# Kernel optimization log

Hardware: AMD Instinct MI355X
Metric: run time of the kernel (lower is better)

Reference implementation:

```python
import jax, jax.numpy as jnp
import numpy as np

N, E, G = 100000, 400000, 4096
H, C = 4, 32            # heads, hidden_dim per head
D_OUT = H * C           # 128
NODE_D, EDGE_D = 38, 13
DEC_H, OUT_D = 64, 1
NEG_SLOPE = 0.2
LN_EPS = 1e-5


def setup_inputs() -> dict:
    key = jax.random.key(0)
    ks = jax.random.split(key, 40)
    r = lambda k, s: jax.random.normal(k, s, jnp.float32) * 0.1
    inp = {
        "x": jax.random.normal(ks[0], (N, NODE_D), jnp.float32),
        "edge_index": jax.random.randint(ks[1], (2, E), 0, N),
        "edge_attr": jax.random.uniform(ks[2], (E, EDGE_D), jnp.float32),
        "batch": jnp.sort(jax.random.randint(ks[3], (N,), 0, G)),
        # --- block 1 (in=38) ---
        "Wl1": r(ks[4], (NODE_D, D_OUT)), "bl1": jnp.zeros((D_OUT,), jnp.float32),
        "Wr1": r(ks[5], (NODE_D, D_OUT)), "br1": jnp.zeros((D_OUT,), jnp.float32),
        "We1": r(ks[6], (EDGE_D, D_OUT)),
        "att1": r(ks[7], (H, C)), "ab1": jnp.zeros((D_OUT,), jnp.float32),
        "ln_g1": jnp.ones((D_OUT,), jnp.float32), "ln_b1": jnp.zeros((D_OUT,), jnp.float32),
        "Wres": r(ks[8], (NODE_D, D_OUT)), "bres": jnp.zeros((D_OUT,), jnp.float32),
        # --- block 2 (in=128, residual = identity) ---
        "Wl2": r(ks[9], (D_OUT, D_OUT)), "bl2": jnp.zeros((D_OUT,), jnp.float32),
        "Wr2": r(ks[10], (D_OUT, D_OUT)), "br2": jnp.zeros((D_OUT,), jnp.float32),
        "We2": r(ks[11], (EDGE_D, D_OUT)),
        "att2": r(ks[12], (H, C)), "ab2": jnp.zeros((D_OUT,), jnp.float32),
        "ln_g2": jnp.ones((D_OUT,), jnp.float32), "ln_b2": jnp.zeros((D_OUT,), jnp.float32),
        # --- readout MLP ---
        "Wd1": r(ks[13], (D_OUT, DEC_H)), "bd1": jnp.zeros((DEC_H,), jnp.float32),
        "Wd2": r(ks[14], (DEC_H, OUT_D)), "bd2": jnp.zeros((OUT_D,), jnp.float32),
    }
    return inp


def _segment_softmax(logits, seg, n):
    m = jax.ops.segment_max(logits, seg, num_segments=n)
    ex = jnp.exp(logits - m[seg])
    s = jax.ops.segment_sum(ex, seg, num_segments=n)
    return ex / s[seg]


def _gatv2(x, src, dst, e_feat, Wl, bl, Wr, br, We, att, ab):
    n = x.shape[0]
    xl = (x @ Wl + bl).reshape(n, H, C)   # source transform
    xr = (x @ Wr + br).reshape(n, H, C)   # target transform
    ee = (e_feat @ We).reshape(-1, H, C)  # edge transform
    z = jax.nn.leaky_relu(xl[src] + xr[dst] + ee, NEG_SLOPE)  # [E,H,C]
    logits = jnp.einsum('ehc,hc->eh', z, att)                 # [E,H]
    alpha = _segment_softmax(logits, dst, n)                  # softmax over target nbhd
    out = jax.ops.segment_sum(xl[src] * alpha[..., None], dst, num_segments=n)
    return out.reshape(n, D_OUT) + ab


def _layernorm(h, g, b):
    mu = jnp.mean(h, -1, keepdims=True)
    d = h - mu
    v = jnp.mean(d * d, -1, keepdims=True)
    return d * jax.lax.rsqrt(v + LN_EPS) * g + b


def reference(x, edge_index, edge_attr, batch,
              Wl1, bl1, Wr1, br1, We1, att1, ab1, ln_g1, ln_b1, Wres, bres,
              Wl2, bl2, Wr2, br2, We2, att2, ab2, ln_g2, ln_b2,
              Wd1, bd1, Wd2, bd2):
    src, dst = edge_index[0], edge_index[1]
    n = x.shape[0]
    # add_self_loops(fill_value='mean'): self-loop edge attr = mean of incoming edge attrs
    deg = jax.ops.segment_sum(jnp.ones((src.shape[0],), x.dtype), dst, num_segments=n)
    loop_attr = jax.ops.segment_sum(edge_attr, dst, num_segments=n) / jnp.clip(deg, 1.0)[:, None]
    nodes = jnp.arange(n)
    src_a = jnp.concatenate([src, nodes])
    dst_a = jnp.concatenate([dst, nodes])
    ea = jnp.concatenate([edge_attr, loop_attr], axis=0)

    # block 1
    h = _gatv2(x, src_a, dst_a, ea, Wl1, bl1, Wr1, br1, We1, att1, ab1)
    h = jax.nn.elu(h)
    h = _layernorm(h + (x @ Wres + bres), ln_g1, ln_b1)
    # block 2 (identity residual)
    h2 = _gatv2(h, src_a, dst_a, ea, Wl2, bl2, Wr2, br2, We2, att2, ab2)
    h2 = jax.nn.elu(h2)
    h2 = _layernorm(h2 + h, ln_g2, ln_b2)

    # global mean pool over graphs
    cnt = jax.ops.segment_sum(jnp.ones((n,), x.dtype), batch, num_segments=G)
    g = jax.ops.segment_sum(h2, batch, num_segments=G) / jnp.clip(cnt, 1.0)[:, None]

    return jax.nn.relu(g @ Wd1 + bd1) @ Wd2 + bd2
```

## Files before the change

### kernel.cpp

```cpp
#include <hip/hip_runtime.h>

typedef unsigned short u16;
typedef unsigned int   u32;
typedef __attribute__((ext_vector_type(8))) short short8;
typedef __attribute__((ext_vector_type(4))) float float4v;
typedef __attribute__((ext_vector_type(2))) float float2v;

#define NODE_D   38
#define EDGE_D   13
#define D_OUT    128
#define NEG_SLOPE 0.2f
#define LN_EPS   1e-5f

__device__ __forceinline__ float bf2f(u16 v) { return __uint_as_float(((u32)v) << 16); }
__device__ __forceinline__ u16 f2bf(float f) {
    u32 u = __float_as_uint(f);
    u += 0x7fffu + ((u >> 16) & 1u);
    return (u16)(u >> 16);
}

__global__ void k_pre(const int* __restrict__ dst, int E, int* __restrict__ deg,
                      const int* __restrict__ batch, int N, int G, int* __restrict__ goff) {
    int i = blockIdx.x * blockDim.x + threadIdx.x;
    if (i < E) atomicAdd(deg + dst[i], 1);
    if (i < N) {
        int b = batch[i];
        int prev = (i == 0) ? -1 : batch[i - 1];
        for (int g = prev + 1; g <= b; g++) goff[g] = i;
        if (i == N - 1)
            for (int g = b + 1; g <= G; g++) goff[g] = N;
    }
}

#define SCAN_CHUNK 1024
__global__ void k_scan1(const int* __restrict__ cnt, int N, int addone, int* __restrict__ bsum) {
    __shared__ int sh[256];
    int base = blockIdx.x * SCAN_CHUNK;
    int t = threadIdx.x;
    int s = 0;
#pragma unroll
    for (int i = 0; i < 4; i++) { int idx = base + t * 4 + i; if (idx < N) s += cnt[idx] + addone; }
    sh[t] = s; __syncthreads();
    for (int ofs = 128; ofs > 0; ofs >>= 1) {
        if (t < ofs) sh[t] += sh[t + ofs];
        __syncthreads();
    }
    if (t == 0) bsum[blockIdx.x] = sh[0];
}
__global__ void k_scan2(const int* __restrict__ bsum, int nb, int* __restrict__ boff) {
    __shared__ int sh[256];
    int t = threadIdx.x;
    if (nb <= 256) {
        int v = (t < nb) ? bsum[t] : 0;
        sh[t] = v; __syncthreads();
        for (int ofs = 1; ofs < 256; ofs <<= 1) {
            int x = (t >= ofs) ? sh[t - ofs] : 0;
            __syncthreads();
            sh[t] += x;
            __syncthreads();
        }
        if (t < nb) boff[t] = sh[t] - v;
        if (t == nb - 1) boff[nb] = sh[t];
    } else if (t == 0) {
        int run = 0;
        for (int i = 0; i < nb; i++) { boff[i] = run; run += bsum[i]; }
        boff[nb] = run;
    }
}
__global__ void k_scan3(const int* __restrict__ cnt, int N, int addone,
                        const int* __restrict__ boff, int nb, int* __restrict__ off) {
    __shared__ int wtot[4];
    int base = blockIdx.x * SCAN_CHUNK;
    int t = threadIdx.x;
    int lane = t & 63, w = t >> 6;
    int v[4]; int s = 0;
#pragma unroll
    for (int i = 0; i < 4; i++) { int idx = base + t * 4 + i; v[i] = (idx < N) ? cnt[idx] + addone : 0; s += v[i]; }
    int inc = s;
#pragma unroll
    for (int ofs = 1; ofs < 64; ofs <<= 1) {
        int x = __shfl_up(inc, ofs, 64);
        if (lane >= ofs) inc += x;
    }
    if (lane == 63) wtot[w] = inc;
    __syncthreads();
    int wofs = 0;
    for (int i = 0; i < w; i++) wofs += wtot[i];
    int run = boff[blockIdx.x] + wofs + (inc - s);
#pragma unroll
    for (int i = 0; i < 4; i++) {
        int idx = base + t * 4 + i;
        if (idx < N) off[idx] = run;
        run += v[i];
    }
    if (blockIdx.x == 0 && t == 0) off[N] = boff[nb];
}

__global__ void k_fill(const int* __restrict__ src, const int* __restrict__ dst,
                       const float* __restrict__ eattr, int E,
                       const int* __restrict__ csr_off, int* __restrict__ fill,
                       int* __restrict__ csr_src, u16* __restrict__ A) {
    int e = blockIdx.x * blockDim.x + threadIdx.x;
    if (e >= E) return;
    int d = dst[e];
    int pos = csr_off[d] + atomicAdd(fill + d, 1);
    csr_src[pos] = src[e];
    u16 row[16];
#pragma unroll
    for (int k = 0; k < EDGE_D; k++) row[k] = f2bf(eattr[(size_t)e * EDGE_D + k]);
#pragma unroll
    for (int k = EDGE_D; k < 16; k++) row[k] = 0;
    uint4* rp = (uint4*)(A + (size_t)pos * 16);
    rp[0] = (uint4){(u32)row[0] | ((u32)row[1] << 16), (u32)row[2] | ((u32)row[3] << 16),
                    (u32)row[4] | ((u32)row[5] << 16), (u32)row[6] | ((u32)row[7] << 16)};
    rp[1] = (uint4){(u32)row[8] | ((u32)row[9] << 16), (u32)row[10] | ((u32)row[11] << 16),
                    (u32)row[12] | ((u32)row[13] << 16), (u32)row[14] | ((u32)row[15] << 16)};
}

__global__ void k_self(const int* __restrict__ csr_off, int N,
                       int* __restrict__ csr_src, u16* __restrict__ A) {
    int tid = blockIdx.x * blockDim.x + threadIdx.x;
    if (tid >= N * 16) return;
    int n = tid >> 4, k = tid & 15;
    int b = csr_off[n], e2 = csr_off[n + 1] - 1;
    u16 v = 0;
    if (k < EDGE_D) {
        float s = 0.f;
        for (int j = b; j < e2; j++) s += bf2f(A[(size_t)j * 16 + k]);
        v = f2bf(s / fmaxf((float)(e2 - b), 1.f));
    }
    A[(size_t)e2 * 16 + k] = v;
    if (k == 0) csr_src[e2] = n;
}

template <int KPAD, int CT, int KREAL, bool IN_BF16>
__global__ __launch_bounds__(256) void k_tf_mfma(
    const void* __restrict__ in_v,
    const float* __restrict__ W0, const float* __restrict__ b0,
    const float* __restrict__ W1, const float* __restrict__ b1,
    const float* __restrict__ W2, const float* __restrict__ b2,
    u16* __restrict__ o0, u16* __restrict__ o1, u16* __restrict__ o2,
    int N) {
    constexpr int RS = KPAD + 8;
    __shared__ u16 Bsw[CT * 16 * RS];
    __shared__ float bsh[CT * 16];
    const float* Ws[3] = {W0, W1, W2};
    const float* bs[3] = {b0, b1, b2};
    u16* outs[3] = {o0, o1, o2};
    int t = threadIdx.x;
    for (int i = t; i < CT * 16 * KPAD; i += 256) {
        int c = i / KPAD, k = i - c * KPAD;
        float v = (k < KREAL) ? Ws[c >> 7][(size_t)k * 128 + (c & 127)] : 0.f;
        Bsw[c * RS + k] = f2bf(v);
    }
    for (int i = t; i < CT * 16; i += 256) bsh[i] = bs[i >> 7][i & 127];
    __syncthreads();

    int wid = t >> 6, lane = t & 63;
    int quad = lane >> 4, m = lane & 15;

    for (int g0 = blockIdx.x * 64; g0 < N; g0 += gridDim.x * 64) {
        int na = g0 + wid * 16 + m;
        if (na > N - 1) na = N - 1;
        short8 a[KPAD / 32];
        if (IN_BF16) {
            const u16* in = (const u16*)in_v;
#pragma unroll
            for (int kc = 0; kc < KPAD / 32; kc++)
                a[kc] = *(const short8*)(in + (size_t)na * KPAD + kc * 32 + quad * 8);
        } else {
            const float* in = (const float*)in_v;
#pragma unroll
            for (int kc = 0; kc < KPAD / 32; kc++)
#pragma unroll
                for (int j = 0; j < 8; j++) {
                    int k = kc * 32 + quad * 8 + j;
                    float v = (k < KREAL) ? in[(size_t)na * KREAL + k] : 0.f;
                    a[kc][j] = (short)f2bf(v);
                }
        }
        float4v acc[CT];
#pragma unroll
        for (int ct = 0; ct < CT; ct++) acc[ct] = (float4v){0.f, 0.f, 0.f, 0.f};
#pragma unroll
        for (int ct = 0; ct < CT; ct++) {
#pragma unroll
            for (int kc = 0; kc < KPAD / 32; kc++) {
                short8 b = *(const short8*)(&Bsw[(ct * 16 + m) * RS + kc * 32 + quad * 8]);
                acc[ct] = __builtin_amdgcn_mfma_f32_16x16x32_bf16(a[kc], b, acc[ct], 0, 0, 0);
            }
        }
#pragma unroll
        for (int ct = 0; ct < CT; ct++) {
            int col = ct * 16 + m;
            u16* op = outs[col >> 7];
            int cc = col & 127;
            float bv = bsh[col];
#pragma unroll
            for (int r = 0; r < 4; r++) {
                int node = g0 + wid * 16 + quad * 4 + r;
                if (node < N) op[(size_t)node * 128 + cc] = f2bf(acc[ct][r] + bv);
            }
        }
    }
}

__global__ __launch_bounds__(256) void k_gat(
    const int* __restrict__ csr_off, const int* __restrict__ csr_src,
    const u16* __restrict__ A_csr,
    const u16* __restrict__ xl, const u16* __restrict__ xr,
    const u16* __restrict__ res, const float* __restrict__ We,
    const float* __restrict__ att, const float* __restrict__ ab,
    const float* __restrict__ lng, const float* __restrict__ lnb,
    u16* __restrict__ hout, int N, int npw) {
    int t = threadIdx.x;
    int wid = t >> 6, lane = t & 63;
    int wave = blockIdx.x * 4 + wid;
    int n0 = wave * npw;
    if (n0 >= N) return;
    int n1 = n0 + npw; if (n1 > N) n1 = N;

    float2v we2[EDGE_D];
#pragma unroll
    for (int k = 0; k < EDGE_D; k++)
        we2[k] = (float2v){We[k * D_OUT + 2 * lane], We[k * D_OUT + 2 * lane + 1]};
    float a0 = att[2 * lane], a1 = att[2 * lane + 1];
    float abv0 = ab[2 * lane], abv1 = ab[2 * lane + 1];
    float lg0 = lng[2 * lane], lg1 = lng[2 * lane + 1];
    float lb0 = lnb[2 * lane], lb1 = lnb[2 * lane + 1];

    const u32* xl32 = (const u32*)xl;
    int wbeg = csr_off[n0];
    int wend = csr_off[n1];
    int cl = wend - 1;

    u32 xw = xl32[(size_t)csr_src[wbeg] * 64 + lane];
    const uint4* ap = (const uint4*)(A_csr + (size_t)wbeg * 16);
    uint4 aq0 = ap[0], aq1 = ap[1];

    int i = wbeg;
    for (int n = n0; n < n1; n++) {
        int end = csr_off[n + 1];
        u32 xrw = ((const u32*)xr)[(size_t)n * 64 + lane];
        float2v xr2 = (float2v){bf2f((u16)(xrw & 0xffff)), bf2f((u16)(xrw >> 16))};

        float ssum = 0.f;
        float2v acc2 = (float2v){0.f, 0.f};
        for (; i < end; i++) {
            u32 xwc = xw;
            uint4 q0 = aq0, q1 = aq1;
            {
                int ip = (i + 1 < wend) ? i + 1 : cl;
                xw = xl32[(size_t)csr_src[ip] * 64 + lane];
                const uint4* ap2 = (const uint4*)(A_csr + (size_t)ip * 16);
                aq0 = ap2[0]; aq1 = ap2[1];
            }
            u32 dw[8] = {q0.x, q0.y, q0.z, q0.w, q1.x, q1.y, q1.z, q1.w};
            float2v ee = (float2v){0.f, 0.f};
#pragma unroll
            for (int k = 0; k < EDGE_D; k++) {
                u32 d = dw[k >> 1];
                float av = bf2f((u16)((k & 1) ? (d >> 16) : (d & 0xffff)));
                ee += we2[k] * av;
            }
            float2v xs = (float2v){bf2f((u16)(xwc & 0xffff)), bf2f((u16)(xwc >> 16))};
            float2v z = xs + xr2 + ee;
            float z0 = z[0], z1 = z[1];
            z0 = (z0 > 0.f) ? z0 : z0 * NEG_SLOPE;
            z1 = (z1 > 0.f) ? z1 : z1 * NEG_SLOPE;
            float p = z0 * a0 + z1 * a1;
            p += __shfl_xor(p, 1, 64);
            p += __shfl_xor(p, 2, 64);
            p += __shfl_xor(p, 4, 64);
            p += __shfl_xor(p, 8, 64);
            float wgt = __expf(p);
            ssum += wgt;
            acc2 += xs * wgt;
        }

        float inv = 1.f / ssum;
        float o0 = acc2[0] * inv + abv0;
        float o1 = acc2[1] * inv + abv1;
        o0 = (o0 > 0.f) ? o0 : (__expf(o0) - 1.f);
        o1 = (o1 > 0.f) ? o1 : (__expf(o1) - 1.f);
        u32 rw = ((const u32*)res)[(size_t)n * 64 + lane];
        o0 += bf2f((u16)(rw & 0xffff));
        o1 += bf2f((u16)(rw >> 16));
        float sm = o0 + o1;
#pragma unroll
        for (int mk = 1; mk < 64; mk <<= 1) sm += __shfl_xor(sm, mk, 64);
        float mu = sm * (1.f / 128.f);
        float d0 = o0 - mu, d1 = o1 - mu;
        float vv = d0 * d0 + d1 * d1;
#pragma unroll
        for (int mk = 1; mk < 64; mk <<= 1) vv += __shfl_xor(vv, mk, 64);
        float rs = rsqrtf(vv * (1.f / 128.f) + LN_EPS);
        float h0 = d0 * rs * lg0 + lb0;
        float h1 = d1 * rs * lg1 + lb1;
        ((u32*)hout)[(size_t)n * 64 + lane] = (u32)f2bf(h0) | ((u32)f2bf(h1) << 16);
    }
}

__global__ __launch_bounds__(128) void k_pool_read(
    const u16* __restrict__ h2, const int* __restrict__ goff,
    const float* __restrict__ Wd1, const float* __restrict__ bd1,
    const float* __restrict__ Wd2, const float* __restrict__ bd2,
    float* __restrict__ out, int G) {
    __shared__ float psh[128];
    __shared__ float rsh[2][64];
    int g = blockIdx.x;
    int c = threadIdx.x;
    int b = goff[g], e = goff[g + 1];
    float s = 0.f;
    for (int n = b; n < e; n++) s += bf2f(h2[(size_t)n * 128 + c]);
    psh[c] = s / fmaxf((float)(e - b), 1.f);
    __syncthreads();
    int j = c & 63, hw = c >> 6;
    float acc = (hw == 0) ? bd1[j] : 0.f;
    int k0 = hw * 64;
    for (int k = k0; k < k0 + 64; k++)
        acc += psh[k] * Wd1[k * 64 + j];
    rsh[hw][j] = acc;
    __syncthreads();
    if (c < 64) {
        float a = fmaxf(rsh[0][c] + rsh[1][c], 0.f);
        float v = a * Wd2[c];
#pragma unroll
        for (int mk = 1; mk < 64; mk <<= 1) v += __shfl_xor(v, mk, 64);
        if (c == 0) out[g] = v + bd2[0];
    }
}

extern "C" void kernel_launch(void* const* d_in, const int* in_sizes, int n_in,
                              void* d_out, int out_size, void* d_ws, size_t ws_size,
                              hipStream_t stream) {
    const float* x     = (const float*)d_in[0];
    const int*   eidx  = (const int*)d_in[1];
    const float* eattr = (const float*)d_in[2];
    const int*   batch = (const int*)d_in[3];
    const float* Wl1 = (const float*)d_in[4],  *bl1 = (const float*)d_in[5];
    const float* Wr1 = (const float*)d_in[6],  *br1 = (const float*)d_in[7];
    const float* We1 = (const float*)d_in[8],  *att1 = (const float*)d_in[9],  *ab1 = (const float*)d_in[10];
    const float* lng1 = (const float*)d_in[11], *lnb1 = (const float*)d_in[12];
    const float* Wres = (const float*)d_in[13], *bres = (const float*)d_in[14];
    const float* Wl2 = (const float*)d_in[15], *bl2 = (const float*)d_in[16];
    const float* Wr2 = (const float*)d_in[17], *br2 = (const float*)d_in[18];
    const float* We2 = (const float*)d_in[19], *att2 = (const float*)d_in[20], *ab2 = (const float*)d_in[21];
    const float* lng2 = (const float*)d_in[22], *lnb2 = (const float*)d_in[23];
    const float* Wd1 = (const float*)d_in[24], *bd1 = (const float*)d_in[25];
    const float* Wd2 = (const float*)d_in[26], *bd2 = (const float*)d_in[27];

    int N = in_sizes[0] / NODE_D;
    int E = in_sizes[1] / 2;
    int G = out_size;
    int EN = E + N;
    const int* src = eidx;
    const int* dst = eidx + E;

    char* w = (char*)d_ws;
    auto alloc = [&](size_t bytes) -> char* {
        char* p = w;
        w += (bytes + 255) & ~(size_t)255;
        return p;
    };
    int NB = (N + SCAN_CHUNK - 1) / SCAN_CHUNK;
    int*   csr_off  = (int*)alloc((size_t)(N + 1) * 4);
    int*   csr_src  = (int*)alloc((size_t)EN * 4);
    u16*   A_csr    = (u16*)alloc((size_t)(EN + 64) * 16 * 2);
    u16*   xlb      = (u16*)alloc((size_t)N * D_OUT * 2);
    u16*   xrb      = (u16*)alloc((size_t)N * D_OUT * 2);
    u16*   resb     = (u16*)alloc((size_t)N * D_OUT * 2);
    u16*   hb       = (u16*)alloc((size_t)N * D_OUT * 2);
    int*   goff     = (int*)alloc((size_t)(G + 1) * 4);
    size_t szN = ((size_t)N * 4 + 255) & ~(size_t)255;
    char*  zp   = alloc(2 * szN);
    int*   deg  = (int*)zp;
    int*   fill = (int*)(zp + szN);
    int*   bsum = (int*)alloc((size_t)(NB + 1) * 4);
    int*   boff = (int*)alloc((size_t)(NB + 1) * 4);

    hipMemsetAsync(zp, 0, 2 * szN, stream);

    int mx = (E > N) ? E : N;
    k_pre<<<(mx + 255) / 256, 256, 0, stream>>>(dst, E, deg, batch, N, G, goff);

    k_scan1<<<NB, 256, 0, stream>>>(deg, N, 1, bsum);
    k_scan2<<<1, 256, 0, stream>>>(bsum, NB, boff);
    k_scan3<<<NB, 256, 0, stream>>>(deg, N, 1, boff, NB, csr_off);
    k_fill<<<(E + 255) / 256, 256, 0, stream>>>(src, dst, eattr, E, csr_off, fill, csr_src, A_csr);
    k_self<<<((size_t)N * 16 + 255) / 256, 256, 0, stream>>>(csr_off, N, csr_src, A_csr);

    int npw = 4;
    int gblocks = (N + npw * 4 - 1) / (npw * 4);

    k_tf_mfma<64, 24, NODE_D, false><<<640, 256, 0, stream>>>(
        x, Wl1, bl1, Wr1, br1, Wres, bres, xlb, xrb, resb, N);
    k_gat<<<gblocks, 256, 0, stream>>>(csr_off, csr_src, A_csr,
                                       xlb, xrb, resb, We1, att1, ab1, lng1, lnb1, hb, N, npw);

    k_tf_mfma<128, 16, 128, true><<<640, 256, 0, stream>>>(
        hb, Wl2, bl2, Wr2, br2, Wr2, br2, xlb, xrb, xrb, N);
    k_gat<<<gblocks, 256, 0, stream>>>(csr_off, csr_src, A_csr,
                                       xlb, xrb, hb, We2, att2, ab2, lng2, lnb2, resb, N, npw);

    k_pool_read<<<G, 128, 0, stream>>>(resb, goff, Wd1, bd1, Wd2, bd2, (float*)d_out, G);
}
```

Before: 577.5 us.

## Compute self-loop edges inline in GAT kernel and slim CSR build

Self-loop edges are no longer stored in the CSR. The GAT kernel now sums the edge projections of each node's incoming edges and uses their mean as the self-loop edge term. Because the edge projection is linear, the mean of projected features stands in for projecting the mean attributes. The separate k_self pass, the scan2 kernel and the fill counter array are removed: scan3 computes its block prefix from the block sums and also writes a mutable offset copy used directly by the fill atomics. This cuts launches and memory traffic, at the cost of a redundant serial block-sum loop in each scan block and slightly different rounding, since the self-loop term is now computed in fp32 rather than from bf16-rounded attribute means.

```diff
diff --git a/kernel.cpp b/kernel.cpp
--- a/kernel.cpp
+++ b/kernel.cpp
@@ -33,13 +33,13 @@
 }
 
 #define SCAN_CHUNK 1024
-__global__ void k_scan1(const int* __restrict__ cnt, int N, int addone, int* __restrict__ bsum) {
+__global__ void k_scan1(const int* __restrict__ cnt, int N, int* __restrict__ bsum) {
     __shared__ int sh[256];
     int base = blockIdx.x * SCAN_CHUNK;
     int t = threadIdx.x;
     int s = 0;
 #pragma unroll
-    for (int i = 0; i < 4; i++) { int idx = base + t * 4 + i; if (idx < N) s += cnt[idx] + addone; }
+    for (int i = 0; i < 4; i++) { int idx = base + t * 4 + i; if (idx < N) s += cnt[idx]; }
     sh[t] = s; __syncthreads();
     for (int ofs = 128; ofs > 0; ofs >>= 1) {
         if (t < ofs) sh[t] += sh[t + ofs];
@@ -47,35 +47,17 @@
     }
     if (t == 0) bsum[blockIdx.x] = sh[0];
 }
-__global__ void k_scan2(const int* __restrict__ bsum, int nb, int* __restrict__ boff) {
-    __shared__ int sh[256];
-    int t = threadIdx.x;
-    if (nb <= 256) {
-        int v = (t < nb) ? bsum[t] : 0;
-        sh[t] = v; __syncthreads();
-        for (int ofs = 1; ofs < 256; ofs <<= 1) {
-            int x = (t >= ofs) ? sh[t - ofs] : 0;
-            __syncthreads();
-            sh[t] += x;
-            __syncthreads();
-        }
-        if (t < nb) boff[t] = sh[t] - v;
-        if (t == nb - 1) boff[nb] = sh[t];
-    } else if (t == 0) {
-        int run = 0;
-        for (int i = 0; i < nb; i++) { boff[i] = run; run += bsum[i]; }
-        boff[nb] = run;
-    }
-}
-__global__ void k_scan3(const int* __restrict__ cnt, int N, int addone,
-                        const int* __restrict__ boff, int nb, int* __restrict__ off) {
+__global__ void k_scan3(const int* __restrict__ cnt, int N, const int* __restrict__ bsum,
+                        int nb, int* __restrict__ off, int* __restrict__ off_mut) {
     __shared__ int wtot[4];
-    int base = blockIdx.x * SCAN_CHUNK;
+    __shared__ int base_sh;
+    int blk = blockIdx.x;
+    int base = blk * SCAN_CHUNK;
     int t = threadIdx.x;
     int lane = t & 63, w = t >> 6;
     int v[4]; int s = 0;
 #pragma unroll
-    for (int i = 0; i < 4; i++) { int idx = base + t * 4 + i; v[i] = (idx < N) ? cnt[idx] + addone : 0; s += v[i]; }
+    for (int i = 0; i < 4; i++) { int idx = base + t * 4 + i; v[i] = (idx < N) ? cnt[idx] : 0; s += v[i]; }
     int inc = s;
 #pragma unroll
     for (int ofs = 1; ofs < 64; ofs <<= 1) {
@@ -83,27 +65,34 @@
         if (lane >= ofs) inc += x;
     }
     if (lane == 63) wtot[w] = inc;
+    if (t < 64) {
+        int b = 0;
+        for (int j = t; j < blk; j += 64) b += bsum[j];
+#pragma unroll
+        for (int mk = 1; mk < 64; mk <<= 1) b += __shfl_xor(b, mk, 64);
+        if (t == 0) base_sh = b;
+    }
     __syncthreads();
     int wofs = 0;
     for (int i = 0; i < w; i++) wofs += wtot[i];
-    int run = boff[blockIdx.x] + wofs + (inc - s);
+    int run = base_sh + wofs + (inc - s);
 #pragma unroll
     for (int i = 0; i < 4; i++) {
         int idx = base + t * 4 + i;
-        if (idx < N) off[idx] = run;
+        if (idx < N) { off[idx] = run; off_mut[idx] = run; }
         run += v[i];
     }
-    if (blockIdx.x == 0 && t == 0) off[N] = boff[nb];
+    if (blk == nb - 1 && t == 255) off[N] = run;
 }
 
 __global__ void k_fill(const int* __restrict__ src, const int* __restrict__ dst,
                        const float* __restrict__ eattr, int E,
-                       const int* __restrict__ csr_off, int* __restrict__ fill,
+                       int* __restrict__ off_mut,
                        int* __restrict__ csr_src, u16* __restrict__ A) {
     int e = blockIdx.x * blockDim.x + threadIdx.x;
     if (e >= E) return;
     int d = dst[e];
-    int pos = csr_off[d] + atomicAdd(fill + d, 1);
+    int pos = atomicAdd(off_mut + d, 1);
     csr_src[pos] = src[e];
     u16 row[16];
 #pragma unroll
@@ -115,22 +104,6 @@
                     (u32)row[4] | ((u32)row[5] << 16), (u32)row[6] | ((u32)row[7] << 16)};
     rp[1] = (uint4){(u32)row[8] | ((u32)row[9] << 16), (u32)row[10] | ((u32)row[11] << 16),
                     (u32)row[12] | ((u32)row[13] << 16), (u32)row[14] | ((u32)row[15] << 16)};
-}
-
-__global__ void k_self(const int* __restrict__ csr_off, int N,
-                       int* __restrict__ csr_src, u16* __restrict__ A) {
-    int tid = blockIdx.x * blockDim.x + threadIdx.x;
-    if (tid >= N * 16) return;
-    int n = tid >> 4, k = tid & 15;
-    int b = csr_off[n], e2 = csr_off[n + 1] - 1;
-    u16 v = 0;
-    if (k < EDGE_D) {
-        float s = 0.f;
-        for (int j = b; j < e2; j++) s += bf2f(A[(size_t)j * 16 + k]);
-        v = f2bf(s / fmaxf((float)(e2 - b), 1.f));
-    }
-    A[(size_t)e2 * 16 + k] = v;
-    if (k == 0) csr_src[e2] = n;
 }
 
 template <int KPAD, int CT, int KREAL, bool IN_BF16>
@@ -234,18 +207,25 @@
     int wend = csr_off[n1];
     int cl = wend - 1;
 
-    u32 xw = xl32[(size_t)csr_src[wbeg] * 64 + lane];
-    const uint4* ap = (const uint4*)(A_csr + (size_t)wbeg * 16);
-    uint4 aq0 = ap[0], aq1 = ap[1];
+    u32 xw = 0;
+    uint4 aq0 = (uint4){0, 0, 0, 0}, aq1 = (uint4){0, 0, 0, 0};
+    if (wbeg < wend) {
+        xw = xl32[(size_t)csr_src[wbeg] * 64 + lane];
+        const uint4* ap = (const uint4*)(A_csr + (size_t)wbeg * 16);
+        aq0 = ap[0]; aq1 = ap[1];
+    }
 
     int i = wbeg;
     for (int n = n0; n < n1; n++) {
         int end = csr_off[n + 1];
+        int nbeg = i;
         u32 xrw = ((const u32*)xr)[(size_t)n * 64 + lane];
         float2v xr2 = (float2v){bf2f((u16)(xrw & 0xffff)), bf2f((u16)(xrw >> 16))};
+        u32 xsw_self = xl32[(size_t)n * 64 + lane];
 
         float ssum = 0.f;
         float2v acc2 = (float2v){0.f, 0.f};
+        float2v eesum = (float2v){0.f, 0.f};
         for (; i < end; i++) {
             u32 xwc = xw;
             uint4 q0 = aq0, q1 = aq1;
@@ -263,8 +243,26 @@
                 float av = bf2f((u16)((k & 1) ? (d >> 16) : (d & 0xffff)));
                 ee += we2[k] * av;
             }
+            eesum += ee;
             float2v xs = (float2v){bf2f((u16)(xwc & 0xffff)), bf2f((u16)(xwc >> 16))};
             float2v z = xs + xr2 + ee;
+            float z0 = z[0], z1 = z[1];
+            z0 = (z0 > 0.f) ? z0 : z0 * NEG_SLOPE;
+            z1 = (z1 > 0.f) ? z1 : z1 * NEG_SLOPE;
+            float p = z0 * a0 + z1 * a1;
+            p += __shfl_xor(p, 1, 64);
+            p += __shfl_xor(p, 2, 64);
+            p += __shfl_xor(p, 4, 64);
+            p += __shfl_xor(p, 8, 64);
+            float wgt = __expf(p);
+            ssum += wgt;
+            acc2 += xs * wgt;
+        }
+
+        {
+            float invd = 1.f / fmaxf((float)(end - nbeg), 1.f);
+            float2v xs = (float2v){bf2f((u16)(xsw_self & 0xffff)), bf2f((u16)(xsw_self >> 16))};
+            float2v z = xs + xr2 + eesum * invd;
             float z0 = z[0], z1 = z[1];
             z0 = (z0 > 0.f) ? z0 : z0 * NEG_SLOPE;
             z1 = (z1 > 0.f) ? z1 : z1 * NEG_SLOPE;
@@ -353,7 +351,6 @@
     int N = in_sizes[0] / NODE_D;
     int E = in_sizes[1] / 2;
     int G = out_size;
-    int EN = E + N;
     const int* src = eidx;
     const int* dst = eidx + E;
 
@@ -365,30 +362,25 @@
     };
     int NB = (N + SCAN_CHUNK - 1) / SCAN_CHUNK;
     int*   csr_off  = (int*)alloc((size_t)(N + 1) * 4);
-    int*   csr_src  = (int*)alloc((size_t)EN * 4);
-    u16*   A_csr    = (u16*)alloc((size_t)(EN + 64) * 16 * 2);
+    int*   off_mut  = (int*)alloc((size_t)(N + 1) * 4);
+    int*   csr_src  = (int*)alloc((size_t)E * 4);
+    u16*   A_csr    = (u16*)alloc((size_t)(E + 64) * 16 * 2);
     u16*   xlb      = (u16*)alloc((size_t)N * D_OUT * 2);
     u16*   xrb      = (u16*)alloc((size_t)N * D_OUT * 2);
     u16*   resb     = (u16*)alloc((size_t)N * D_OUT * 2);
     u16*   hb       = (u16*)alloc((size_t)N * D_OUT * 2);
     int*   goff     = (int*)alloc((size_t)(G + 1) * 4);
-    size_t szN = ((size_t)N * 4 + 255) & ~(size_t)255;
-    char*  zp   = alloc(2 * szN);
-    int*   deg  = (int*)zp;
-    int*   fill = (int*)(zp + szN);
-    int*   bsum = (int*)alloc((size_t)(NB + 1) * 4);
-    int*   boff = (int*)alloc((size_t)(NB + 1) * 4);
-
-    hipMemsetAsync(zp, 0, 2 * szN, stream);
+    int*   deg      = (int*)alloc((size_t)N * 4);
+    int*   bsum     = (int*)alloc((size_t)(NB + 1) * 4);
+
+    hipMemsetAsync(deg, 0, (size_t)N * 4, stream);
 
     int mx = (E > N) ? E : N;
     k_pre<<<(mx + 255) / 256, 256, 0, stream>>>(dst, E, deg, batch, N, G, goff);
 
-    k_scan1<<<NB, 256, 0, stream>>>(deg, N, 1, bsum);
-    k_scan2<<<1, 256, 0, stream>>>(bsum, NB, boff);
-    k_scan3<<<NB, 256, 0, stream>>>(deg, N, 1, boff, NB, csr_off);
-    k_fill<<<(E + 255) / 256, 256, 0, stream>>>(src, dst, eattr, E, csr_off, fill, csr_src, A_csr);
-    k_self<<<((size_t)N * 16 + 255) / 256, 256, 0, stream>>>(csr_off, N, csr_src, A_csr);
+    k_scan1<<<NB, 256, 0, stream>>>(deg, N, bsum);
+    k_scan3<<<NB, 256, 0, stream>>>(deg, N, bsum, NB, csr_off, off_mut);
+    k_fill<<<(E + 255) / 256, 256, 0, stream>>>(src, dst, eattr, E, off_mut, csr_src, A_csr);
 
     int npw = 4;
     int gblocks = (N + npw * 4 - 1) / (npw * 4);
```

After: 583.9 us. About the same (+1.1%).
